# Performance work log

Measured on AMD Instinct MI355X. Metric: run time of the kernel, lower is better.

Reference implementation:

```python
import jax, jax.numpy as jnp
import numpy as np

DIM = 1024
NUM_HEADS = 16
HEAD_DIM = DIM // NUM_HEADS
SCALE = HEAD_DIM ** -0.5
B, S = 2, 2048


def setup_inputs() -> dict:
    key = jax.random.key(0)
    ks = jax.random.split(key, 5)
    inv = 1.0 / np.sqrt(DIM)  # mimic nn.Linear init scale
    return {
        "query": jax.random.normal(ks[0], (B, S, DIM), dtype=jnp.float32),
        "Wq": jax.random.normal(ks[1], (DIM, DIM), dtype=jnp.float32) * inv,
        "Wk": jax.random.normal(ks[2], (DIM, DIM), dtype=jnp.float32) * inv,
        "Wv": jax.random.normal(ks[3], (DIM, DIM), dtype=jnp.float32) * inv,
        "Wo": jax.random.normal(ks[4], (DIM, DIM), dtype=jnp.float32) * inv,
    }


def reference(query, Wq, Wk, Wv, Wo):
    # nn.Linear(dim, dim, bias=False): y = x @ W.T  (W is [out, in])
    Q = query @ Wq.T  # [B, S, D]
    K = query @ Wk.T
    V = query @ Wv.T
    # split heads: [B, H, S, hd]
    def split(x):
        return x.reshape(B, S, NUM_HEADS, HEAD_DIM).transpose(0, 2, 1, 3)
    Qh, Kh, Vh = split(Q), split(K), split(V)
    scores = jnp.einsum("bhqd,bhkd->bhqk", Qh, Kh) * SCALE  # [B,H,Sq,Sk]
    probs = jax.nn.softmax(scores, axis=-1)
    attn = jnp.einsum("bhqk,bhkd->bhqd", probs, Vh)  # [B,H,Sq,hd]
    attn = attn.transpose(0, 2, 1, 3).reshape(B, S, DIM)
    return attn @ Wo.T
```

## Files before the change

kernel.cpp:

```cpp
#include <hip/hip_runtime.h>
#include <hip/hip_bf16.h>


#define DIMK   1024
#define NHEADS 16
#define HDIM   64
#define BATCH  2
#define SEQ    2048
#define MTOT   (BATCH*SEQ)

typedef __attribute__((ext_vector_type(8))) short bf16x8;
typedef __attribute__((ext_vector_type(4))) float f32x4;

__device__ __forceinline__ void gl16(const void* g, void* l) {
  __builtin_amdgcn_global_load_lds((const __attribute__((address_space(1))) void*)g,
                                   (__attribute__((address_space(3))) void*)l, 16, 0, 0);
}

__device__ __forceinline__ unsigned short f2bf(float f) {
  union { float f; unsigned int u; } a; a.f = f;
  unsigned int r = a.u + 0x7fffu + ((a.u >> 16) & 1u);
  return (unsigned short)(r >> 16);
}
__device__ __forceinline__ float bf2f(unsigned short h) {
  union { unsigned int u; float f; } a; a.u = ((unsigned int)h) << 16;
  return a.f;
}
__device__ __forceinline__ void split2(float v, unsigned short& hi, unsigned short& lo) {
  hi = f2bf(v);
  lo = f2bf(v - bf2f(hi));
}
__device__ __forceinline__ void split2t(float v, unsigned short& hi, unsigned short& lo) {
  union { float f; unsigned int u; } a; a.f = v;
  hi = (unsigned short)(a.u >> 16);
  lo = f2bf(v - bf2f(hi));
}

__global__ __launch_bounds__(256) void convert_kernel(
    const float* __restrict__ X, const float* __restrict__ Wq,
    const float* __restrict__ Wk, const float* __restrict__ Wv,
    const float* __restrict__ Wo,
    unsigned short* __restrict__ Xhi, unsigned short* __restrict__ Xlo,
    unsigned short* __restrict__ Whi, unsigned short* __restrict__ Wlo,
    unsigned short* __restrict__ Wohi, unsigned short* __restrict__ Wolo)
{
  const int NX4 = MTOT * DIMK / 4;
  const int NW4 = DIMK * DIMK / 4;
  int id = blockIdx.x * blockDim.x + threadIdx.x;
  const float4* s; unsigned short* dh; unsigned short* dl; int si, di;
  if (id < NX4) { s = (const float4*)X; si = id; di = id; dh = Xhi; dl = Xlo; }
  else if (id < NX4 + 3 * NW4) {
    int t = id - NX4; di = t;
    if (t < NW4)          { s = (const float4*)Wq; si = t; }
    else if (t < 2 * NW4) { s = (const float4*)Wk; si = t - NW4; }
    else                  { s = (const float4*)Wv; si = t - 2 * NW4; }
    dh = Whi; dl = Wlo;
  } else {
    int t = id - NX4 - 3 * NW4; s = (const float4*)Wo; si = t; di = t; dh = Wohi; dl = Wolo;
  }
  float4 v = s[si];
  ushort4 hi, lo;
  split2(v.x, hi.x, lo.x); split2(v.y, hi.y, lo.y);
  split2(v.z, hi.z, lo.z); split2(v.w, hi.w, lo.w);
  ((ushort4*)dh)[di] = hi;
  ((ushort4*)dl)[di] = lo;
}

__device__ __forceinline__ void gemm_mainloop(
    const unsigned short* __restrict__ Ahi, const unsigned short* __restrict__ Alo,
    const unsigned short* __restrict__ Bhi, const unsigned short* __restrict__ Blo,
    int m0, int n0, int K, unsigned short* As, unsigned short* Bs, f32x4 acc[4][4])
{
  int tid = threadIdx.x; int w = tid >> 6; int l = tid & 63;
  int wm = w >> 1, wn = w & 1, lr = l & 15, lg = l >> 4;
  for (int kk = 0; kk < K; kk += 32) {
#pragma unroll
    for (int it = 0; it < 2; ++it) {
      int c = it * 256 + w * 64 + l;
      int row = c >> 2, col = (c & 3) * 8;
      int lb = (it * 256 + w * 64) * 8;
      gl16(Ahi + (long)(m0 + row) * K + kk + col, As + lb);
      gl16(Alo + (long)(m0 + row) * K + kk + col, As + 4096 + lb);
      gl16(Bhi + (long)(n0 + row) * K + kk + col, Bs + lb);
      gl16(Blo + (long)(n0 + row) * K + kk + col, Bs + 4096 + lb);
    }
    __syncthreads();
    bf16x8 ah[4], al[4], bh[4], bl[4];
#pragma unroll
    for (int i = 0; i < 4; i++) {
      int ra = (wm * 64 + i * 16 + lr) * 32 + lg * 8;
      ah[i] = *(const bf16x8*)(As + ra);
      al[i] = *(const bf16x8*)(As + 4096 + ra);
      int rb = (wn * 64 + i * 16 + lr) * 32 + lg * 8;
      bh[i] = *(const bf16x8*)(Bs + rb);
      bl[i] = *(const bf16x8*)(Bs + 4096 + rb);
    }
#pragma unroll
    for (int mi = 0; mi < 4; mi++)
#pragma unroll
      for (int ni = 0; ni < 4; ni++) {
        acc[mi][ni] = __builtin_amdgcn_mfma_f32_16x16x32_bf16(ah[mi], bh[ni], acc[mi][ni], 0, 0, 0);
        acc[mi][ni] = __builtin_amdgcn_mfma_f32_16x16x32_bf16(ah[mi], bl[ni], acc[mi][ni], 0, 0, 0);
        acc[mi][ni] = __builtin_amdgcn_mfma_f32_16x16x32_bf16(al[mi], bh[ni], acc[mi][ni], 0, 0, 0);
      }
    __syncthreads();
  }
}

__global__ __launch_bounds__(256) void gemm_qkv_kernel(
    const unsigned short* __restrict__ Xhi, const unsigned short* __restrict__ Xlo,
    const unsigned short* __restrict__ Whi, const unsigned short* __restrict__ Wlo,
    unsigned short* __restrict__ Qhi, unsigned short* __restrict__ Qlo,
    unsigned short* __restrict__ Khi, unsigned short* __restrict__ Klo,
    unsigned short* __restrict__ Vthi, unsigned short* __restrict__ Vtlo)
{
  __shared__ __align__(16) unsigned short As[2 * 4096];
  __shared__ __align__(16) unsigned short Bs[2 * 4096];
  int m0 = blockIdx.y * 128, n0 = blockIdx.x * 128;
  f32x4 acc[4][4] = {};
  gemm_mainloop(Xhi, Xlo, Whi, Wlo, m0, n0, DIMK, As, Bs, acc);
  int tid = threadIdx.x; int w = tid >> 6, l = tid & 63;
  int wm = w >> 1, wn = w & 1, lr = l & 15, lg = l >> 4;
  int sec = n0 >> 10;
  int nl = (n0 & 1023) + wn * 64;
#pragma unroll
  for (int mi = 0; mi < 4; mi++) {
    int rbase = m0 + wm * 64 + mi * 16 + lg * 4;
#pragma unroll
    for (int ni = 0; ni < 4; ni++) {
      int col = nl + ni * 16 + lr;
      if (sec == 2) {
        ushort4 hi4, lo4;
        split2(acc[mi][ni][0], hi4.x, lo4.x);
        split2(acc[mi][ni][1], hi4.y, lo4.y);
        split2(acc[mi][ni][2], hi4.z, lo4.z);
        split2(acc[mi][ni][3], hi4.w, lo4.w);
        *(ushort4*)(Vthi + (long)col * MTOT + rbase) = hi4;
        *(ushort4*)(Vtlo + (long)col * MTOT + rbase) = lo4;
      } else {
        unsigned short* dh = (sec == 0) ? Qhi : Khi;
        unsigned short* dl = (sec == 0) ? Qlo : Klo;
        float sc = (sec == 0) ? (0.125f * 1.44269504088896340736f) : 1.0f;
#pragma unroll
        for (int r = 0; r < 4; r++) {
          float v = acc[mi][ni][r] * sc;
          unsigned short h_, l_;
          split2(v, h_, l_);
          dh[(long)(rbase + r) * DIMK + col] = h_;
          dl[(long)(rbase + r) * DIMK + col] = l_;
        }
      }
    }
  }
}

__global__ __launch_bounds__(256) void attn_kernel(
    const unsigned short* __restrict__ Qhi, const unsigned short* __restrict__ Qlo,
    const unsigned short* __restrict__ Khi, const unsigned short* __restrict__ Klo,
    const unsigned short* __restrict__ Vthi, const unsigned short* __restrict__ Vtlo,
    unsigned short* __restrict__ Ahi, unsigned short* __restrict__ Alo)
{
  __shared__ __align__(16) unsigned short Ks[2][2 * 4096];
  __shared__ __align__(16) unsigned short Vs[2][2 * 4096];
  __shared__ __align__(16) unsigned short Ps[2 * 4096];
  int tid = threadIdx.x, w = tid >> 6, l = tid & 63, lr = l & 15, lg = l >> 4;
  int q0 = blockIdx.x * 64;
  int bh = blockIdx.y, b = bh >> 4, h = bh & 15;
  long rowbase = (long)b * SEQ;

  bf16x8 qh[2], ql[2];
#pragma unroll
  for (int ks = 0; ks < 2; ks++) {
    long g = (rowbase + q0 + w * 16 + lr) * DIMK + h * HDIM + ks * 32 + lg * 8;
    qh[ks] = *(const bf16x8*)(Qhi + g);
    ql[ks] = *(const bf16x8*)(Qlo + g);
  }
  bf16x8 ones;
#pragma unroll
  for (int i = 0; i < 8; i++) ones[i] = (short)0x3F80;

  f32x4 o[4] = {};
  f32x4 o1 = {};

  auto stage = [&](int kt, int buf) {
#pragma unroll
    for (int it = 0; it < 2; it++) {
      int c = it * 256 + w * 64 + l;
      int row = c >> 3;
      int col = ((c & 7) ^ (row & 7)) * 8;
      int lb = (it * 256 + w * 64) * 8;
      long gk = (rowbase + kt * 64 + row) * DIMK + h * HDIM + col;
      gl16(Khi + gk, Ks[buf] + lb);
      gl16(Klo + gk, Ks[buf] + 4096 + lb);
      long gv = (long)(h * HDIM + row) * MTOT + rowbase + kt * 64 + col;
      gl16(Vthi + gv, Vs[buf] + lb);
      gl16(Vtlo + gv, Vs[buf] + 4096 + lb);
    }
  };

  stage(0, 0);
  __syncthreads();

  const int NT = SEQ / 64;
  for (int kt = 0; kt < NT; kt++) {
    int cur = kt & 1;
    if (kt + 1 < NT) stage(kt + 1, cur ^ 1);

    const unsigned short* Kb = Ks[cur];
    const unsigned short* Vb = Vs[cur];

    f32x4 s[4] = {};
    __builtin_amdgcn_s_setprio(1);
#pragma unroll
    for (int n = 0; n < 4; n++) {
#pragma unroll
      for (int ks = 0; ks < 2; ks++) {
        int kr = n * 16 + lr;
        int rb = kr * 64 + (((ks * 4 + lg) ^ (kr & 7)) * 8);
        bf16x8 kbh = *(const bf16x8*)(Kb + rb);
        bf16x8 kbl = *(const bf16x8*)(Kb + 4096 + rb);
        s[n] = __builtin_amdgcn_mfma_f32_16x16x32_bf16(qh[ks], kbh, s[n], 0, 0, 0);
        s[n] = __builtin_amdgcn_mfma_f32_16x16x32_bf16(qh[ks], kbl, s[n], 0, 0, 0);
        s[n] = __builtin_amdgcn_mfma_f32_16x16x32_bf16(ql[ks], kbh, s[n], 0, 0, 0);
      }
    }
    __builtin_amdgcn_s_setprio(0);

#pragma unroll
    for (int r = 0; r < 4; r++) {
      int qr = w * 16 + lg * 4 + r;
#pragma unroll
      for (int n = 0; n < 4; n++) {
        float p = exp2f(s[n][r]);
        unsigned short h_, l_;
        split2t(p, h_, l_);
        int addr = qr * 64 + ((n * 16 + lr) ^ ((qr & 7) << 3));
        Ps[addr] = h_; Ps[4096 + addr] = l_;
      }
    }

    __builtin_amdgcn_s_setprio(1);
#pragma unroll
    for (int ks = 0; ks < 2; ks++) {
      int qr = w * 16 + lr;
      int pa = qr * 64 + ((ks * 32 + lg * 8) ^ ((qr & 7) << 3));
      bf16x8 ph = *(const bf16x8*)(Ps + pa);
      bf16x8 pl = *(const bf16x8*)(Ps + 4096 + pa);
      o1 = __builtin_amdgcn_mfma_f32_16x16x32_bf16(ph, ones, o1, 0, 0, 0);
      o1 = __builtin_amdgcn_mfma_f32_16x16x32_bf16(pl, ones, o1, 0, 0, 0);
#pragma unroll
      for (int nd = 0; nd < 4; nd++) {
        int vr = nd * 16 + lr;
        int vb = vr * 64 + (((ks * 4 + lg) ^ (vr & 7)) * 8);
        bf16x8 vh = *(const bf16x8*)(Vb + vb);
        bf16x8 vl = *(const bf16x8*)(Vb + 4096 + vb);
        o[nd] = __builtin_amdgcn_mfma_f32_16x16x32_bf16(ph, vh, o[nd], 0, 0, 0);
        o[nd] = __builtin_amdgcn_mfma_f32_16x16x32_bf16(ph, vl, o[nd], 0, 0, 0);
        o[nd] = __builtin_amdgcn_mfma_f32_16x16x32_bf16(pl, vh, o[nd], 0, 0, 0);
      }
    }
    __builtin_amdgcn_s_setprio(0);
    __syncthreads();
  }

#pragma unroll
  for (int r = 0; r < 4; r++) {
    float inv = 1.0f / o1[r];
#pragma unroll
    for (int nd = 0; nd < 4; nd++) {
      long row = rowbase + q0 + w * 16 + lg * 4 + r;
      int col = h * HDIM + nd * 16 + lr;
      float v = o[nd][r] * inv;
      unsigned short h_, l_;
      split2(v, h_, l_);
      Ahi[row * DIMK + col] = h_;
      Alo[row * DIMK + col] = l_;
    }
  }
}

__global__ __launch_bounds__(256) void gemm_out_kernel(
    const unsigned short* __restrict__ Ahi_, const unsigned short* __restrict__ Alo_,
    const unsigned short* __restrict__ Wohi, const unsigned short* __restrict__ Wolo,
    float* __restrict__ out)
{
  __shared__ __align__(16) unsigned short As[2 * 4096];
  __shared__ __align__(16) unsigned short Bs[2 * 4096];
  int m0 = blockIdx.y * 128, n0 = blockIdx.x * 128;
  f32x4 acc[4][4] = {};
  gemm_mainloop(Ahi_, Alo_, Wohi, Wolo, m0, n0, DIMK, As, Bs, acc);
  int tid = threadIdx.x; int w = tid >> 6, l = tid & 63;
  int wm = w >> 1, wn = w & 1, lr = l & 15, lg = l >> 4;
#pragma unroll
  for (int mi = 0; mi < 4; mi++) {
    int rbase = m0 + wm * 64 + mi * 16 + lg * 4;
#pragma unroll
    for (int ni = 0; ni < 4; ni++) {
      int col = n0 + wn * 64 + ni * 16 + lr;
#pragma unroll
      for (int r = 0; r < 4; r++)
        out[(long)(rbase + r) * DIMK + col] = acc[mi][ni][r];
    }
  }
}

extern "C" void kernel_launch(void* const* d_in, const int* in_sizes, int n_in,
                              void* d_out, int out_size, void* d_ws, size_t ws_size,
                              hipStream_t stream)
{
  const float* X  = (const float*)d_in[0];
  const float* Wq = (const float*)d_in[1];
  const float* Wk = (const float*)d_in[2];
  const float* Wv = (const float*)d_in[3];
  const float* Wo = (const float*)d_in[4];
  float* out = (float*)d_out;
  char* ws = (char*)d_ws;
  const size_t MB = 1u << 20;
  unsigned short* Xhi  = (unsigned short*)(ws + 0 * MB);
  unsigned short* Xlo  = (unsigned short*)(ws + 8 * MB);
  unsigned short* Whi  = (unsigned short*)(ws + 16 * MB);
  unsigned short* Wlo  = (unsigned short*)(ws + 22 * MB);
  unsigned short* Wohi = (unsigned short*)(ws + 28 * MB);
  unsigned short* Wolo = (unsigned short*)(ws + 30 * MB);
  unsigned short* Qhi  = (unsigned short*)(ws + 32 * MB);
  unsigned short* Qlo  = (unsigned short*)(ws + 40 * MB);
  unsigned short* Khi  = (unsigned short*)(ws + 48 * MB);
  unsigned short* Klo  = (unsigned short*)(ws + 56 * MB);
  unsigned short* Vthi = (unsigned short*)(ws + 64 * MB);
  unsigned short* Vtlo = (unsigned short*)(ws + 72 * MB);
  unsigned short* AThi = Xhi;
  unsigned short* ATlo = Xlo;

  convert_kernel<<<8192, 256, 0, stream>>>(X, Wq, Wk, Wv, Wo, Xhi, Xlo, Whi, Wlo, Wohi, Wolo);
  gemm_qkv_kernel<<<dim3(24, 32), 256, 0, stream>>>(Xhi, Xlo, Whi, Wlo,
                                                    Qhi, Qlo, Khi, Klo, Vthi, Vtlo);
  attn_kernel<<<dim3(32, 32), 256, 0, stream>>>(Qhi, Qlo, Khi, Klo, Vthi, Vtlo, AThi, ATlo);
  gemm_out_kernel<<<dim3(8, 32), 256, 0, stream>>>(AThi, ATlo, Wohi, Wolo, out);
}
```

Before: 361.6 us.

## Switch attention to 32x32 MFMA with transposed scores kept in registers

The attention kernel now uses 32x32x16 bf16 MFMAs and computes S transposed (K as the A operand, Q as B), so each lane's score outputs line up with the P operand layout of the PV product. The P tile no longer round-trips through shared memory and the Ps buffer is removed. Each block now covers 128 query rows (32 per wave) with half as many blocks, so every K/V tile staged in LDS is reused by twice as many queries. In exchange, V fragments are gathered from two 4-element LDS reads per operand, register pressure rises, and fewer blocks are available to fill the GPU.

```diff
diff --git a/kernel.cpp b/kernel.cpp
--- a/kernel.cpp
+++ b/kernel.cpp
@@ -10,7 +10,9 @@
 #define MTOT   (BATCH*SEQ)
 
 typedef __attribute__((ext_vector_type(8))) short bf16x8;
+typedef __attribute__((ext_vector_type(4))) short bf16x4;
 typedef __attribute__((ext_vector_type(4))) float f32x4;
+typedef __attribute__((ext_vector_type(16))) float f32x16;
 
 __device__ __forceinline__ void gl16(const void* g, void* l) {
   __builtin_amdgcn_global_load_lds((const __attribute__((address_space(1))) void*)g,
@@ -162,25 +164,24 @@
 {
   __shared__ __align__(16) unsigned short Ks[2][2 * 4096];
   __shared__ __align__(16) unsigned short Vs[2][2 * 4096];
-  __shared__ __align__(16) unsigned short Ps[2 * 4096];
-  int tid = threadIdx.x, w = tid >> 6, l = tid & 63, lr = l & 15, lg = l >> 4;
-  int q0 = blockIdx.x * 64;
+  int tid = threadIdx.x, w = tid >> 6, l = tid & 63, lh = l >> 5, lc = l & 31;
+  int q0 = blockIdx.x * 128;
   int bh = blockIdx.y, b = bh >> 4, h = bh & 15;
   long rowbase = (long)b * SEQ;
 
-  bf16x8 qh[2], ql[2];
-#pragma unroll
-  for (int ks = 0; ks < 2; ks++) {
-    long g = (rowbase + q0 + w * 16 + lr) * DIMK + h * HDIM + ks * 32 + lg * 8;
-    qh[ks] = *(const bf16x8*)(Qhi + g);
-    ql[ks] = *(const bf16x8*)(Qlo + g);
+  bf16x8 qbh[4], qbl[4];
+#pragma unroll
+  for (int kd = 0; kd < 4; kd++) {
+    long g = (rowbase + q0 + w * 32 + lc) * DIMK + h * HDIM + kd * 16 + lh * 8;
+    qbh[kd] = *(const bf16x8*)(Qhi + g);
+    qbl[kd] = *(const bf16x8*)(Qlo + g);
   }
   bf16x8 ones;
 #pragma unroll
   for (int i = 0; i < 8; i++) ones[i] = (short)0x3F80;
 
-  f32x4 o[4] = {};
-  f32x4 o1 = {};
+  f32x16 o[2] = {};
+  f32x16 osum = {};
 
   auto stage = [&](int kt, int buf) {
 #pragma unroll
@@ -209,68 +210,74 @@
     const unsigned short* Kb = Ks[cur];
     const unsigned short* Vb = Vs[cur];
 
-    f32x4 s[4] = {};
-    __builtin_amdgcn_s_setprio(1);
-#pragma unroll
-    for (int n = 0; n < 4; n++) {
-#pragma unroll
-      for (int ks = 0; ks < 2; ks++) {
-        int kr = n * 16 + lr;
-        int rb = kr * 64 + (((ks * 4 + lg) ^ (kr & 7)) * 8);
-        bf16x8 kbh = *(const bf16x8*)(Kb + rb);
-        bf16x8 kbl = *(const bf16x8*)(Kb + 4096 + rb);
-        s[n] = __builtin_amdgcn_mfma_f32_16x16x32_bf16(qh[ks], kbh, s[n], 0, 0, 0);
-        s[n] = __builtin_amdgcn_mfma_f32_16x16x32_bf16(qh[ks], kbl, s[n], 0, 0, 0);
-        s[n] = __builtin_amdgcn_mfma_f32_16x16x32_bf16(ql[ks], kbh, s[n], 0, 0, 0);
+#pragma unroll
+    for (int kg = 0; kg < 2; kg++) {
+      f32x16 s = {};
+      __builtin_amdgcn_s_setprio(1);
+#pragma unroll
+      for (int kd = 0; kd < 4; kd++) {
+        int krow = kg * 32 + lc;
+        int ca = ((2 * kd + lh) ^ (krow & 7)) * 8;
+        bf16x8 kh = *(const bf16x8*)(Kb + krow * 64 + ca);
+        bf16x8 kl = *(const bf16x8*)(Kb + 4096 + krow * 64 + ca);
+        s = __builtin_amdgcn_mfma_f32_32x32x16_bf16(kh, qbh[kd], s, 0, 0, 0);
+        s = __builtin_amdgcn_mfma_f32_32x32x16_bf16(kh, qbl[kd], s, 0, 0, 0);
+        s = __builtin_amdgcn_mfma_f32_32x32x16_bf16(kl, qbh[kd], s, 0, 0, 0);
       }
-    }
-    __builtin_amdgcn_s_setprio(0);
-
-#pragma unroll
-    for (int r = 0; r < 4; r++) {
-      int qr = w * 16 + lg * 4 + r;
-#pragma unroll
-      for (int n = 0; n < 4; n++) {
-        float p = exp2f(s[n][r]);
-        unsigned short h_, l_;
-        split2t(p, h_, l_);
-        int addr = qr * 64 + ((n * 16 + lr) ^ ((qr & 7) << 3));
-        Ps[addr] = h_; Ps[4096 + addr] = l_;
+      __builtin_amdgcn_s_setprio(0);
+
+      bf16x8 pah[2], pal[2];
+#pragma unroll
+      for (int ks2 = 0; ks2 < 2; ks2++)
+#pragma unroll
+        for (int j = 0; j < 8; j++) {
+          float p = exp2f(s[8 * ks2 + j]);
+          unsigned short h_, l_;
+          split2t(p, h_, l_);
+          pah[ks2][j] = (short)h_; pal[ks2][j] = (short)l_;
+        }
+
+      __builtin_amdgcn_s_setprio(1);
+#pragma unroll
+      for (int ks2 = 0; ks2 < 2; ks2++) {
+        osum = __builtin_amdgcn_mfma_f32_32x32x16_bf16(pah[ks2], ones, osum, 0, 0, 0);
+        osum = __builtin_amdgcn_mfma_f32_32x32x16_bf16(pal[ks2], ones, osum, 0, 0, 0);
+#pragma unroll
+        for (int dg = 0; dg < 2; dg++) {
+          int vrow = dg * 32 + lc;
+          int sw = vrow & 7;
+          int c0 = 4 * kg + 2 * ks2;
+          const unsigned short* vb0 = Vb + vrow * 64 + ((c0 ^ sw) * 8) + 4 * lh;
+          const unsigned short* vb1 = Vb + vrow * 64 + (((c0 + 1) ^ sw) * 8) + 4 * lh;
+          bf16x4 vh0 = *(const bf16x4*)vb0;
+          bf16x4 vh1 = *(const bf16x4*)vb1;
+          bf16x4 vl0 = *(const bf16x4*)(vb0 + 4096);
+          bf16x4 vl1 = *(const bf16x4*)(vb1 + 4096);
+          bf16x8 bvh, bvl;
+#pragma unroll
+          for (int jj = 0; jj < 4; jj++) {
+            bvh[jj] = vh0[jj]; bvh[4 + jj] = vh1[jj];
+            bvl[jj] = vl0[jj]; bvl[4 + jj] = vl1[jj];
+          }
+          o[dg] = __builtin_amdgcn_mfma_f32_32x32x16_bf16(pah[ks2], bvh, o[dg], 0, 0, 0);
+          o[dg] = __builtin_amdgcn_mfma_f32_32x32x16_bf16(pah[ks2], bvl, o[dg], 0, 0, 0);
+          o[dg] = __builtin_amdgcn_mfma_f32_32x32x16_bf16(pal[ks2], bvh, o[dg], 0, 0, 0);
+        }
       }
-    }
-
-    __builtin_amdgcn_s_setprio(1);
-#pragma unroll
-    for (int ks = 0; ks < 2; ks++) {
-      int qr = w * 16 + lr;
-      int pa = qr * 64 + ((ks * 32 + lg * 8) ^ ((qr & 7) << 3));
-      bf16x8 ph = *(const bf16x8*)(Ps + pa);
-      bf16x8 pl = *(const bf16x8*)(Ps + 4096 + pa);
-      o1 = __builtin_amdgcn_mfma_f32_16x16x32_bf16(ph, ones, o1, 0, 0, 0);
-      o1 = __builtin_amdgcn_mfma_f32_16x16x32_bf16(pl, ones, o1, 0, 0, 0);
-#pragma unroll
-      for (int nd = 0; nd < 4; nd++) {
-        int vr = nd * 16 + lr;
-        int vb = vr * 64 + (((ks * 4 + lg) ^ (vr & 7)) * 8);
-        bf16x8 vh = *(const bf16x8*)(Vb + vb);
-        bf16x8 vl = *(const bf16x8*)(Vb + 4096 + vb);
-        o[nd] = __builtin_amdgcn_mfma_f32_16x16x32_bf16(ph, vh, o[nd], 0, 0, 0);
-        o[nd] = __builtin_amdgcn_mfma_f32_16x16x32_bf16(ph, vl, o[nd], 0, 0, 0);
-        o[nd] = __builtin_amdgcn_mfma_f32_16x16x32_bf16(pl, vh, o[nd], 0, 0, 0);
-      }
-    }
-    __builtin_amdgcn_s_setprio(0);
+      __builtin_amdgcn_s_setprio(0);
+    }
     __syncthreads();
   }
 
 #pragma unroll
-  for (int r = 0; r < 4; r++) {
-    float inv = 1.0f / o1[r];
-#pragma unroll
-    for (int nd = 0; nd < 4; nd++) {
-      long row = rowbase + q0 + w * 16 + lg * 4 + r;
-      int col = h * HDIM + nd * 16 + lr;
-      float v = o[nd][r] * inv;
+  for (int r = 0; r < 16; r++) {
+    int qlocal = (r & 3) + 8 * (r >> 2) + 4 * lh;
+    long row = rowbase + q0 + w * 32 + qlocal;
+    float inv = 1.0f / osum[r];
+#pragma unroll
+    for (int dg = 0; dg < 2; dg++) {
+      int col = h * HDIM + dg * 32 + lc;
+      float v = o[dg][r] * inv;
       unsigned short h_, l_;
       split2(v, h_, l_);
       Ahi[row * DIMK + col] = h_;
@@ -334,6 +341,6 @@
   convert_kernel<<<8192, 256, 0, stream>>>(X, Wq, Wk, Wv, Wo, Xhi, Xlo, Whi, Wlo, Wohi, Wolo);
   gemm_qkv_kernel<<<dim3(24, 32), 256, 0, stream>>>(Xhi, Xlo, Whi, Wlo,
                                                     Qhi, Qlo, Khi, Klo, Vthi, Vtlo);
-  attn_kernel<<<dim3(32, 32), 256, 0, stream>>>(Qhi, Qlo, Khi, Klo, Vthi, Vtlo, AThi, ATlo);
+  attn_kernel<<<dim3(16, 32), 256, 0, stream>>>(Qhi, Qlo, Khi, Klo, Vthi, Vtlo, AThi, ATlo);
   gemm_out_kernel<<<dim3(8, 32), 256, 0, stream>>>(AThi, ATlo, Wohi, Wolo, out);
 }
```

Result: faster. 349.7 us (-3.3%).
